# Kernel tuning notes

Hardware: AMD Instinct MI355X
Metric: run time of the kernel (lower is better)

## Reference

```python
import jax, jax.numpy as jnp
import numpy as np

B, S, D = 4, 1024, 1024
H, DK = 16, 64

def setup_inputs() -> dict:
    key = jax.random.key(0)
    ks = jax.random.split(key, 12)
    s = lambda k, shape, scale: (jax.random.normal(k, shape, dtype=jnp.float32) * scale)
    inp = {
        "query": s(ks[0], (B, S, D), 1.0),
        "key":   s(ks[1], (B, S, D), 1.0),
        "value": s(ks[2], (B, S, D), 1.0),
        # per-head query projections stacked: [H, D, DK]
        "Wq": s(ks[3], (H, D, DK), D ** -0.5),
        "bq": jnp.zeros((H, DK), jnp.float32),
        # shared key / value projections (MQA)
        "Wk": s(ks[4], (D, DK), D ** -0.5),
        "bk": jnp.zeros((DK,), jnp.float32),
        "Wv": s(ks[5], (D, DK), D ** -0.5),
        "bv": jnp.zeros((DK,), jnp.float32),
        # combine_heads: Dense(key_dim) applied to concat of H head outputs
        "Wc": s(ks[6], (H * DK, DK), (H * DK) ** -0.5),
        "bc": jnp.zeros((DK,), jnp.float32),
    }
    return inp


def reference(query, key, value, Wq, bq, Wk, bk, Wv, bv, Wc, bc):
    # per-head query projections, batched over heads: [B,H,S,DK]
    q = jnp.einsum('bsd,hdk->bhsk', query, Wq) + bq[None, :, None, :]
    # shared K/V (multi-query attention): [B,S,DK]
    k = jnp.einsum('bsd,dk->bsk', key, Wk) + bk
    v = jnp.einsum('bsd,dk->bsk', value, Wv) + bv
    scale = 1.0 / jnp.sqrt(jnp.asarray(DK, q.dtype))
    # scores: [B,H,S,S], K broadcast across heads
    scores = jnp.einsum('bhsk,btk->bhst', q, k) * scale
    attn = jax.nn.softmax(scores, axis=-1)
    # head outputs: [B,H,S,DK]
    out_h = jnp.einsum('bhst,btk->bhsk', attn, v)
    # concat heads along last axis (head order preserved): [B,S,H*DK]
    concat = out_h.transpose(0, 2, 1, 3).reshape(B, S, H * DK)
    output = concat @ Wc + bc  # [B,S,DK]; dropout=0.0 -> identity
    return output, attn
```

## Files before the change

kernel.cpp:

```cpp
#include <hip/hip_runtime.h>

typedef __bf16 bf16;
typedef __attribute__((ext_vector_type(4))) float f32x4;
typedef __attribute__((ext_vector_type(8))) bf16 bf16x8;
typedef __attribute__((ext_vector_type(4))) bf16 bf16x4;

constexpr int Bc = 4, Sc = 1024, Dc = 1024, Hc = 16, DKc = 64;


__device__ __forceinline__ void stage64(bf16* s, const void* g, int ld, int f32src) {
  const int t = threadIdx.x;
#pragma unroll
  for (int i = 0; i < 2; ++i) {
    const int G = t + i * 256;
    const int r = G >> 3, gr = G & 7;
    bf16x8 o;
    if (f32src) {
      const float* gp = (const float*)g + (long)r * ld + gr * 8;
      const f32x4 a = *(const f32x4*)gp;
      const f32x4 b = *(const f32x4*)(gp + 4);
      o[0]=(bf16)a[0]; o[1]=(bf16)a[1]; o[2]=(bf16)a[2]; o[3]=(bf16)a[3];
      o[4]=(bf16)b[0]; o[5]=(bf16)b[1]; o[6]=(bf16)b[2]; o[7]=(bf16)b[3];
    } else {
      o = *(const bf16x8*)((const bf16*)g + (long)r * ld + gr * 8);
    }
    *(bf16x8*)(s + r * 64 + ((gr * 8) ^ ((r & 7) << 3))) = o;
  }
}

__device__ __forceinline__ bf16x8 frag_ld(const bf16* s, int row, int kofs) {
  const int lane = threadIdx.x & 63;
  const int c0 = kofs + (((lane >> 4) & 3) << 2);
  const int sw = (row & 7) << 3;
  union { bf16x8 v8; bf16x4 v4[2]; } u;
  u.v4[0] = *(const bf16x4*)(s + row * 64 + (c0 ^ sw));
  u.v4[1] = *(const bf16x4*)(s + row * 64 + ((c0 + 16) ^ sw));
  return u.v8;
}

__device__ __forceinline__ void gld16(const bf16* g, bf16* l) {
  __builtin_amdgcn_global_load_lds(
      (const __attribute__((address_space(1))) void*)g,
      (__attribute__((address_space(3))) void*)l, 16, 0, 0);
}

#define WAIT_BAR(vm) do { \
  asm volatile("s_waitcnt vmcnt(" vm ")" ::: "memory"); \
  __builtin_amdgcn_s_barrier(); \
  __builtin_amdgcn_sched_barrier(0); } while (0)

__global__ __launch_bounds__(256) void transpose_weights(
    const float* __restrict__ Wq, const float* __restrict__ Wk,
    const float* __restrict__ Wv, const float* __restrict__ Wc,
    bf16* __restrict__ WqT, bf16* __restrict__ WkT,
    bf16* __restrict__ WvT, bf16* __restrict__ WcT) {
  const int bid = blockIdx.x;
  const float* src; bf16* dst; float scl; int r0;
  if (bid < 256)      { const int hh = bid >> 4; r0 = (bid & 15) * 64;
                        src = Wq + (hh << 16); dst = WqT + (hh << 16); scl = 0.125f; }
  else if (bid < 272) { r0 = (bid - 256) * 64; src = Wk; dst = WkT; scl = 1.f; }
  else if (bid < 288) { r0 = (bid - 272) * 64; src = Wv; dst = WvT; scl = 1.f; }
  else                { r0 = (bid - 288) * 64; src = Wc; dst = WcT; scl = 1.f; }

  __shared__ float tile[64][68];
  const int t = threadIdx.x;
  const int rr = t >> 4, cc = (t & 15) * 4;
#pragma unroll
  for (int i = 0; i < 4; ++i) {
    const f32x4 v = *(const f32x4*)(src + (long)(r0 + rr + i * 16) * 64 + cc);
    *(f32x4*)(&tile[rr + i * 16][cc]) = v;
  }
  __syncthreads();
#pragma unroll
  for (int i = 0; i < 2; ++i) {
    const int g = t + i * 256, orow = g >> 3, oc = (g & 7) * 8;
    bf16x8 o;
#pragma unroll
    for (int jj = 0; jj < 8; ++jj) o[jj] = (bf16)(tile[oc + jj][orow] * scl);
    *(bf16x8*)(dst + (long)orow * 1024 + r0 + oc) = o;
  }
}

__global__ __launch_bounds__(256) void proj_kernel(
    const float* __restrict__ query, const float* __restrict__ key,
    const float* __restrict__ value, const bf16* __restrict__ WqT,
    const bf16* __restrict__ WkT, const bf16* __restrict__ WvT,
    const float* __restrict__ bq, const float* __restrict__ bk,
    const float* __restrict__ bv, bf16* __restrict__ q_cat,
    bf16* __restrict__ k_proj, bf16* __restrict__ vTp) {
  const int bid = blockIdx.x;
  const void* A; const void* BT; bf16* C; const float* bias;
  int m0, n0, ldA, ldBT, ldC, aF32, bF32, biasM;
  float bscale;
  if (bid < 1024) {
    m0 = (bid >> 4) << 6; n0 = (bid & 15) << 6;
    A = query; ldA = 1024; aF32 = 1;
    BT = WqT;  ldBT = 1024; bF32 = 0;
    C = q_cat; ldC = 1024; bias = bq; biasM = 0; bscale = 0.125f;
  } else if (bid < 1088) {
    m0 = (bid - 1024) << 6; n0 = 0;
    A = key;    ldA = 1024; aF32 = 1;
    BT = WkT;   ldBT = 1024; bF32 = 0;
    C = k_proj; ldC = 64; bias = bk; biasM = 0; bscale = 1.f;
  } else {
    const int j = bid - 1088;
    m0 = 0; n0 = (j & 15) << 6;
    A = WvT; ldA = 1024; aF32 = 0;
    BT = value + ((long)(j >> 4) << 20); ldBT = 1024; bF32 = 1;
    C = vTp + ((long)(j >> 4) << 16); ldC = 1024; bias = bv; biasM = 1; bscale = 1.f;
  }

  __shared__ bf16 sA[2][4096];
  __shared__ bf16 sB[2][4096];
  const int lane = threadIdx.x & 63;
  const int w = threadIdx.x >> 6;

  f32x4 acc[4];
#pragma unroll
  for (int nb = 0; nb < 4; ++nb) acc[nb] = (f32x4){0.f, 0.f, 0.f, 0.f};

  stage64(sA[0], aF32 ? (const void*)((const float*)A + (long)m0 * ldA)
                      : (const void*)((const bf16*)A + (long)m0 * ldA), ldA, aF32);
  stage64(sB[0], bF32 ? (const void*)((const float*)BT + (long)n0 * ldBT)
                      : (const void*)((const bf16*)BT + (long)n0 * ldBT), ldBT, bF32);
  __syncthreads();

  for (int it = 0; it < 16; ++it) {
    const int p = it & 1;
    if (it < 15) {
      const int kk = (it + 1) * 64;
      stage64(sA[p ^ 1], aF32 ? (const void*)((const float*)A + (long)m0 * ldA + kk)
                              : (const void*)((const bf16*)A + (long)m0 * ldA + kk), ldA, aF32);
      stage64(sB[p ^ 1], bF32 ? (const void*)((const float*)BT + (long)n0 * ldBT + kk)
                              : (const void*)((const bf16*)BT + (long)n0 * ldBT + kk), ldBT, bF32);
    }
#pragma unroll
    for (int ks = 0; ks < 2; ++ks) {
      const bf16x8 af = frag_ld(sA[p], 16 * w + (lane & 15), ks * 32);
#pragma unroll
      for (int nb = 0; nb < 4; ++nb) {
        const bf16x8 bfr = frag_ld(sB[p], nb * 16 + (lane & 15), ks * 32);
        acc[nb] = __builtin_amdgcn_mfma_f32_16x16x32_bf16(af, bfr, acc[nb], 0, 0, 0);
      }
    }
    __syncthreads();
  }

  const int rbase = m0 + 16 * w + ((lane >> 4) << 2);
#pragma unroll
  for (int nb = 0; nb < 4; ++nb) {
    const int col = n0 + nb * 16 + (lane & 15);
    const float bn = biasM ? 0.f : bias[col] * bscale;
#pragma unroll
    for (int r = 0; r < 4; ++r) {
      const int row = rbase + r;
      C[(long)row * ldC + col] = (bf16)(acc[nb][r] + (biasM ? bias[row] : bn));
    }
  }
}

__global__ __launch_bounds__(256) void combine_kernel(
    const bf16* __restrict__ concat, const bf16* __restrict__ WcT,
    float* __restrict__ part) {
  const int ks = blockIdx.x >> 6;
  const int m0 = (blockIdx.x & 63) * 64;
  const int k0 = ks * 256;
  __shared__ bf16 sA[2][4096];
  __shared__ bf16 sB[2][4096];
  const int lane = threadIdx.x & 63;
  const int w = threadIdx.x >> 6;

  f32x4 acc[4];
#pragma unroll
  for (int nb = 0; nb < 4; ++nb) acc[nb] = (f32x4){0.f, 0.f, 0.f, 0.f};

  stage64(sA[0], concat + (long)m0 * 1024 + k0, 1024, 0);
  stage64(sB[0], WcT + k0, 1024, 0);
  __syncthreads();
  for (int it = 0; it < 4; ++it) {
    const int p = it & 1;
    if (it < 3) {
      const int kk = k0 + (it + 1) * 64;
      stage64(sA[p ^ 1], concat + (long)m0 * 1024 + kk, 1024, 0);
      stage64(sB[p ^ 1], WcT + kk, 1024, 0);
    }
#pragma unroll
    for (int ksl = 0; ksl < 2; ++ksl) {
      const bf16x8 af = frag_ld(sA[p], 16 * w + (lane & 15), ksl * 32);
#pragma unroll
      for (int nb = 0; nb < 4; ++nb) {
        const bf16x8 bfr = frag_ld(sB[p], nb * 16 + (lane & 15), ksl * 32);
        acc[nb] = __builtin_amdgcn_mfma_f32_16x16x32_bf16(af, bfr, acc[nb], 0, 0, 0);
      }
    }
    __syncthreads();
  }
  const int rbase = m0 + 16 * w + ((lane >> 4) << 2);
  float* pb = part + (long)ks * 262144;
#pragma unroll
  for (int nb = 0; nb < 4; ++nb) {
    const int col = nb * 16 + (lane & 15);
#pragma unroll
    for (int r = 0; r < 4; ++r)
      pb[(long)(rbase + r) * 64 + col] = acc[nb][r];
  }
}

__global__ __launch_bounds__(256) void reduce_combine(
    const float* __restrict__ part, const float* __restrict__ bc,
    float* __restrict__ out0) {
  const int i = blockIdx.x * 256 + threadIdx.x;
  out0[i] = part[i] + part[i + 262144] + part[i + 524288] + part[i + 786432]
          + bc[i & 63];
}

__global__ __launch_bounds__(128) void attn_kernel(
    const bf16* __restrict__ q_cat, const bf16* __restrict__ k_proj,
    const bf16* __restrict__ vT, float* __restrict__ attn_out,
    bf16* __restrict__ concat) {
  const int s0 = blockIdx.x * 64;
  const int h = blockIdx.y, b = blockIdx.z;
  const int t = threadIdx.x;
  const int lane = t & 63;
  const int w = t >> 6;

  __shared__ bf16 sK[2][4096];
  __shared__ bf16 sV[2][4096];

  const bf16* kp = k_proj + (long)b * Sc * DKc;
  const bf16* vp = vT + (long)b * DKc * Sc;
  float* ao = attn_out + ((long)(b * Hc + h) * Sc + s0) * Sc;
  bf16* co = concat + (long)(b * Sc + s0) * (Hc * DKc) + h * DKc;

  const int c0q = (lane >> 4) << 2;
  const int wq0 = w * 32;

  const int rloc = t >> 3;
  const int col8 = ((t & 7) ^ (rloc & 7)) << 3;
  const int ldsw = w << 9;

  auto stageK = [&](int pb, int tt) {
#pragma unroll
    for (int c = 0; c < 4; ++c)
      gld16(kp + ((long)tt << 12) + (c * 16 + rloc) * 64 + col8,
            &sK[pb][c * 1024 + ldsw]);
  };
  auto stageV = [&](int pb, int tt) {
#pragma unroll
    for (int c = 0; c < 4; ++c)
      gld16(vp + (long)(c * 16 + rloc) * 1024 + tt * 64 + col8,
            &sV[pb][c * 1024 + ldsw]);
  };

  bf16x8 qf[2][2];
#pragma unroll
  for (int qg = 0; qg < 2; ++qg) {
    const bf16* qrow = q_cat + (long)(b * Sc + s0 + wq0 + qg * 16 + (lane & 15)) * 1024 + h * 64;
    union { bf16x8 v8; bf16x4 v4[2]; } a, c;
    a.v4[0] = *(const bf16x4*)(qrow + c0q);
    a.v4[1] = *(const bf16x4*)(qrow + c0q + 16);
    c.v4[0] = *(const bf16x4*)(qrow + c0q + 32);
    c.v4[1] = *(const bf16x4*)(qrow + c0q + 48);
    qf[qg][0] = a.v8; qf[qg][1] = c.v8;
  }

  stageK(0, 0);
  WAIT_BAR("0");
  float lsum[2] = {0.f, 0.f};
  for (int tc = 0; tc < 16; ++tc) {
    const int p = tc & 1;
    if (tc < 15) stageK(p ^ 1, tc + 1);
    bf16x8 kf[2][4];
#pragma unroll
    for (int ks = 0; ks < 2; ++ks)
#pragma unroll
      for (int nb = 0; nb < 4; ++nb)
        kf[ks][nb] = frag_ld(sK[p], nb * 16 + (lane & 15), ks * 32);
#pragma unroll
    for (int qg = 0; qg < 2; ++qg) {
      f32x4 sc[4];
#pragma unroll
      for (int nb = 0; nb < 4; ++nb) sc[nb] = (f32x4){0.f, 0.f, 0.f, 0.f};
#pragma unroll
      for (int ks = 0; ks < 2; ++ks)
#pragma unroll
        for (int nb = 0; nb < 4; ++nb)
          sc[nb] = __builtin_amdgcn_mfma_f32_16x16x32_bf16(kf[ks][nb], qf[qg][ks], sc[nb], 0, 0, 0);
#pragma unroll
      for (int nb = 0; nb < 4; ++nb)
#pragma unroll
        for (int r = 0; r < 4; ++r) lsum[qg] += __expf(sc[nb][r]);
    }
    if (tc < 15) WAIT_BAR("0");
  }

#pragma unroll
  for (int qg = 0; qg < 2; ++qg) {
    lsum[qg] += __shfl_xor(lsum[qg], 16, 64);
    lsum[qg] += __shfl_xor(lsum[qg], 32, 64);
  }
  const float invl0 = 1.f / lsum[0], invl1 = 1.f / lsum[1];

  f32x4 oacc[2][4];
#pragma unroll
  for (int qg = 0; qg < 2; ++qg)
#pragma unroll
    for (int nb = 0; nb < 4; ++nb) oacc[qg][nb] = (f32x4){0.f, 0.f, 0.f, 0.f};

  stageK(0, 0);
  stageV(0, 0);
  WAIT_BAR("0");
  for (int tc = 0; tc < 16; ++tc) {
    const int p = tc & 1;
    if (tc < 15) { stageK(p ^ 1, tc + 1); stageV(p ^ 1, tc + 1); }
    bf16x8 kf[2][4];
#pragma unroll
    for (int ks = 0; ks < 2; ++ks)
#pragma unroll
      for (int nb = 0; nb < 4; ++nb)
        kf[ks][nb] = frag_ld(sK[p], nb * 16 + (lane & 15), ks * 32);
    bf16x8 pa[2][2];
#pragma unroll
    for (int qg = 0; qg < 2; ++qg) {
      f32x4 sc[4];
#pragma unroll
      for (int nb = 0; nb < 4; ++nb) sc[nb] = (f32x4){0.f, 0.f, 0.f, 0.f};
#pragma unroll
      for (int ks = 0; ks < 2; ++ks)
#pragma unroll
        for (int nb = 0; nb < 4; ++nb)
          sc[nb] = __builtin_amdgcn_mfma_f32_16x16x32_bf16(kf[ks][nb], qf[qg][ks], sc[nb], 0, 0, 0);
      const float invl = qg ? invl1 : invl0;
      float* aobase = ao + (long)(wq0 + qg * 16 + (lane & 15)) * Sc + tc * 64 + c0q;
      float e[4][4];
#pragma unroll
      for (int nb = 0; nb < 4; ++nb) {
#pragma unroll
        for (int r = 0; r < 4; ++r) e[nb][r] = __expf(sc[nb][r]);
        f32x4 av;
#pragma unroll
        for (int r = 0; r < 4; ++r) av[r] = e[nb][r] * invl;
        *(f32x4*)(aobase + nb * 16) = av;
      }
#pragma unroll
      for (int ks = 0; ks < 2; ++ks)
#pragma unroll
        for (int jj = 0; jj < 4; ++jj) {
          pa[qg][ks][jj]     = (bf16)e[2 * ks][jj];
          pa[qg][ks][4 + jj] = (bf16)e[2 * ks + 1][jj];
        }
    }
#pragma unroll
    for (int ks = 0; ks < 2; ++ks)
#pragma unroll
      for (int nb = 0; nb < 4; ++nb) {
        const bf16x8 vf = frag_ld(sV[p], nb * 16 + (lane & 15), ks * 32);
        oacc[0][nb] = __builtin_amdgcn_mfma_f32_16x16x32_bf16(pa[0][ks], vf, oacc[0][nb], 0, 0, 0);
        oacc[1][nb] = __builtin_amdgcn_mfma_f32_16x16x32_bf16(pa[1][ks], vf, oacc[1][nb], 0, 0, 0);
      }
    if (tc < 15) WAIT_BAR("8");
  }

#pragma unroll
  for (int qg = 0; qg < 2; ++qg) {
    const float invl = qg ? invl1 : invl0;
    float invo[4];
#pragma unroll
    for (int r = 0; r < 4; ++r) invo[r] = __shfl(invl, c0q + r, 64);
#pragma unroll
    for (int nb = 0; nb < 4; ++nb) {
#pragma unroll
      for (int r = 0; r < 4; ++r) {
        const int row = wq0 + qg * 16 + c0q + r;
        const int col = nb * 16 + (lane & 15);
        co[(long)row * (Hc * DKc) + col] = (bf16)(oacc[qg][nb][r] * invo[r]);
      }
    }
  }
}


extern "C" void kernel_launch(void* const* d_in, const int* in_sizes, int n_in,
                              void* d_out, int out_size, void* d_ws, size_t ws_size,
                              hipStream_t stream) {
  const float* query = (const float*)d_in[0];
  const float* key   = (const float*)d_in[1];
  const float* value = (const float*)d_in[2];
  const float* Wq = (const float*)d_in[3];
  const float* bq = (const float*)d_in[4];
  const float* Wk = (const float*)d_in[5];
  const float* bk = (const float*)d_in[6];
  const float* Wv = (const float*)d_in[7];
  const float* bv = (const float*)d_in[8];
  const float* Wc = (const float*)d_in[9];
  const float* bc = (const float*)d_in[10];

  bf16* WqT    = (bf16*)d_ws;
  bf16* WkT    = WqT + 1048576;
  bf16* WvT    = WkT + 65536;
  bf16* WcT    = WvT + 65536;
  bf16* q_cat  = WcT + 65536;
  bf16* k_proj = q_cat + 4194304;
  bf16* vTp    = k_proj + 262144;
  bf16* concat = vTp + 262144;
  float* part  = (float*)(concat + 4194304);

  float* out0 = (float*)d_out;
  float* attn = out0 + (long)Bc * Sc * DKc;

  transpose_weights<<<304, 256, 0, stream>>>(Wq, Wk, Wv, Wc, WqT, WkT, WvT, WcT);

  proj_kernel<<<1152, 256, 0, stream>>>(query, key, value, WqT, WkT, WvT,
                                        bq, bk, bv, q_cat, k_proj, vTp);

  attn_kernel<<<dim3(16, 16, 4), 128, 0, stream>>>(q_cat, k_proj, vTp, attn, concat);

  combine_kernel<<<256, 256, 0, stream>>>(concat, WcT, part);
  reduce_combine<<<1024, 256, 0, stream>>>(part, bc, out0);
}
```

Baseline: 188.2 us.

## Load K/V fragments directly from global and use exp2 with folded scale

Removes the LDS double-buffered staging of K and V in the attention kernel. Each wave now reads its MFMA fragments straight from global memory, which eliminates barriers and shared memory. The loops are fully unrolled so the loads can be scheduled early. The softmax exponent switches to the hardware exp2, with log2(e) folded into the query scale, which saves a multiply per element. The trade-off is that every wave re-reads K/V through cache instead of sharing one staged copy, and the loads are narrow 8-byte reads.

```diff
diff --git a/kernel.cpp b/kernel.cpp
--- a/kernel.cpp
+++ b/kernel.cpp
@@ -6,6 +6,8 @@
 typedef __attribute__((ext_vector_type(4))) bf16 bf16x4;
 
 constexpr int Bc = 4, Sc = 1024, Dc = 1024, Hc = 16, DKc = 64;
+#define ESCALE 0.18033688011112042f
+#define EXP2F(x) __builtin_amdgcn_exp2f(x)
 
 
 __device__ __forceinline__ void stage64(bf16* s, const void* g, int ld, int f32src) {
@@ -38,16 +40,15 @@
   return u.v8;
 }
 
-__device__ __forceinline__ void gld16(const bf16* g, bf16* l) {
-  __builtin_amdgcn_global_load_lds(
-      (const __attribute__((address_space(1))) void*)g,
-      (__attribute__((address_space(3))) void*)l, 16, 0, 0);
-}
-
-#define WAIT_BAR(vm) do { \
-  asm volatile("s_waitcnt vmcnt(" vm ")" ::: "memory"); \
-  __builtin_amdgcn_s_barrier(); \
-  __builtin_amdgcn_sched_barrier(0); } while (0)
+__device__ __forceinline__ bf16x8 gfrag(const bf16* base, long ld, int row, int kofs) {
+  const int lane = threadIdx.x & 63;
+  const int c0 = kofs + (((lane >> 4) & 3) << 2);
+  const bf16* p = base + (long)row * ld + c0;
+  union { bf16x8 v8; bf16x4 v4[2]; } u;
+  u.v4[0] = *(const bf16x4*)(p);
+  u.v4[1] = *(const bf16x4*)(p + 16);
+  return u.v8;
+}
 
 __global__ __launch_bounds__(256) void transpose_weights(
     const float* __restrict__ Wq, const float* __restrict__ Wk,
@@ -57,7 +58,7 @@
   const int bid = blockIdx.x;
   const float* src; bf16* dst; float scl; int r0;
   if (bid < 256)      { const int hh = bid >> 4; r0 = (bid & 15) * 64;
-                        src = Wq + (hh << 16); dst = WqT + (hh << 16); scl = 0.125f; }
+                        src = Wq + (hh << 16); dst = WqT + (hh << 16); scl = ESCALE; }
   else if (bid < 272) { r0 = (bid - 256) * 64; src = Wk; dst = WkT; scl = 1.f; }
   else if (bid < 288) { r0 = (bid - 272) * 64; src = Wv; dst = WvT; scl = 1.f; }
   else                { r0 = (bid - 288) * 64; src = Wc; dst = WcT; scl = 1.f; }
@@ -96,7 +97,7 @@
     m0 = (bid >> 4) << 6; n0 = (bid & 15) << 6;
     A = query; ldA = 1024; aF32 = 1;
     BT = WqT;  ldBT = 1024; bF32 = 0;
-    C = q_cat; ldC = 1024; bias = bq; biasM = 0; bscale = 0.125f;
+    C = q_cat; ldC = 1024; bias = bq; biasM = 0; bscale = ESCALE;
   } else if (bid < 1088) {
     m0 = (bid - 1024) << 6; n0 = 0;
     A = key;    ldA = 1024; aF32 = 1;
@@ -224,9 +225,6 @@
   const int lane = t & 63;
   const int w = t >> 6;
 
-  __shared__ bf16 sK[2][4096];
-  __shared__ bf16 sV[2][4096];
-
   const bf16* kp = k_proj + (long)b * Sc * DKc;
   const bf16* vp = vT + (long)b * DKc * Sc;
   float* ao = attn_out + ((long)(b * Hc + h) * Sc + s0) * Sc;
@@ -234,23 +232,6 @@
 
   const int c0q = (lane >> 4) << 2;
   const int wq0 = w * 32;
-
-  const int rloc = t >> 3;
-  const int col8 = ((t & 7) ^ (rloc & 7)) << 3;
-  const int ldsw = w << 9;
-
-  auto stageK = [&](int pb, int tt) {
-#pragma unroll
-    for (int c = 0; c < 4; ++c)
-      gld16(kp + ((long)tt << 12) + (c * 16 + rloc) * 64 + col8,
-            &sK[pb][c * 1024 + ldsw]);
-  };
-  auto stageV = [&](int pb, int tt) {
-#pragma unroll
-    for (int c = 0; c < 4; ++c)
-      gld16(vp + (long)(c * 16 + rloc) * 1024 + tt * 64 + col8,
-            &sV[pb][c * 1024 + ldsw]);
-  };
 
   bf16x8 qf[2][2];
 #pragma unroll
@@ -264,18 +245,15 @@
     qf[qg][0] = a.v8; qf[qg][1] = c.v8;
   }
 
-  stageK(0, 0);
-  WAIT_BAR("0");
   float lsum[2] = {0.f, 0.f};
+#pragma unroll
   for (int tc = 0; tc < 16; ++tc) {
-    const int p = tc & 1;
-    if (tc < 15) stageK(p ^ 1, tc + 1);
     bf16x8 kf[2][4];
 #pragma unroll
     for (int ks = 0; ks < 2; ++ks)
 #pragma unroll
       for (int nb = 0; nb < 4; ++nb)
-        kf[ks][nb] = frag_ld(sK[p], nb * 16 + (lane & 15), ks * 32);
+        kf[ks][nb] = gfrag(kp, 64, tc * 64 + nb * 16 + (lane & 15), ks * 32);
 #pragma unroll
     for (int qg = 0; qg < 2; ++qg) {
       f32x4 sc[4];
@@ -289,9 +267,8 @@
 #pragma unroll
       for (int nb = 0; nb < 4; ++nb)
 #pragma unroll
-        for (int r = 0; r < 4; ++r) lsum[qg] += __expf(sc[nb][r]);
-    }
-    if (tc < 15) WAIT_BAR("0");
+        for (int r = 0; r < 4; ++r) lsum[qg] += EXP2F(sc[nb][r]);
+    }
   }
 
 #pragma unroll
@@ -307,18 +284,14 @@
 #pragma unroll
     for (int nb = 0; nb < 4; ++nb) oacc[qg][nb] = (f32x4){0.f, 0.f, 0.f, 0.f};
 
-  stageK(0, 0);
-  stageV(0, 0);
-  WAIT_BAR("0");
+#pragma unroll
   for (int tc = 0; tc < 16; ++tc) {
-    const int p = tc & 1;
-    if (tc < 15) { stageK(p ^ 1, tc + 1); stageV(p ^ 1, tc + 1); }
     bf16x8 kf[2][4];
 #pragma unroll
     for (int ks = 0; ks < 2; ++ks)
 #pragma unroll
       for (int nb = 0; nb < 4; ++nb)
-        kf[ks][nb] = frag_ld(sK[p], nb * 16 + (lane & 15), ks * 32);
+        kf[ks][nb] = gfrag(kp, 64, tc * 64 + nb * 16 + (lane & 15), ks * 32);
     bf16x8 pa[2][2];
 #pragma unroll
     for (int qg = 0; qg < 2; ++qg) {
@@ -336,7 +309,7 @@
 #pragma unroll
       for (int nb = 0; nb < 4; ++nb) {
 #pragma unroll
-        for (int r = 0; r < 4; ++r) e[nb][r] = __expf(sc[nb][r]);
+        for (int r = 0; r < 4; ++r) e[nb][r] = EXP2F(sc[nb][r]);
         f32x4 av;
 #pragma unroll
         for (int r = 0; r < 4; ++r) av[r] = e[nb][r] * invl;
@@ -354,11 +327,10 @@
     for (int ks = 0; ks < 2; ++ks)
 #pragma unroll
       for (int nb = 0; nb < 4; ++nb) {
-        const bf16x8 vf = frag_ld(sV[p], nb * 16 + (lane & 15), ks * 32);
+        const bf16x8 vf = gfrag(vp, 1024, nb * 16 + (lane & 15), tc * 64 + ks * 32);
         oacc[0][nb] = __builtin_amdgcn_mfma_f32_16x16x32_bf16(pa[0][ks], vf, oacc[0][nb], 0, 0, 0);
         oacc[1][nb] = __builtin_amdgcn_mfma_f32_16x16x32_bf16(pa[1][ks], vf, oacc[1][nb], 0, 0, 0);
       }
-    if (tc < 15) WAIT_BAR("8");
   }
 
 #pragma unroll
```

Result: slower. 290.6 us (+54.4%).
